# Kernel optimization log

Measured on AMD Instinct MI355X. Metric: run time of the kernel, lower is better.

## Reference

```python
import jax, jax.numpy as jnp
import numpy as np

B, S, D, H = 2, 2048, 1024, 16
DK = D // H
LARGE = 1e9
LN_EPS = 1e-5


def sinusoidal_embeddings(seq_len, d):
    pos = jnp.arange(seq_len, dtype=jnp.float32)[:, None]          # [S,1]
    i = jnp.arange(d // 2, dtype=jnp.float32)[None, :]             # [1,d/2]
    freq = jnp.exp(-(2.0 * i / d) * jnp.log(10000.0))
    ang = pos * freq                                               # [S,d/2]
    pe = jnp.zeros((seq_len, d), dtype=jnp.float32)
    pe = pe.at[:, 0::2].set(jnp.sin(ang))
    pe = pe.at[:, 1::2].set(jnp.cos(ang))
    return pe


def setup_inputs() -> dict:
    key = jax.random.key(0)
    ks = jax.random.split(key, 6)
    sc = 1.0 / np.sqrt(D)
    return {
        "X": jax.random.normal(ks[0], (B, S, D), jnp.float32),
        "W_q": jax.random.normal(ks[1], (D, D), jnp.float32) * sc,
        "W_k": jax.random.normal(ks[2], (D, D), jnp.float32) * sc,
        "W_v": jax.random.normal(ks[3], (D, D), jnp.float32) * sc,
        "W_o": jax.random.normal(ks[4], (D, D), jnp.float32) * sc,
        "alpha": jnp.ones((1, H, S - 1, 1), jnp.float32),
        "ln_scale": jnp.ones((D,), jnp.float32),
        "ln_bias": jnp.zeros((D,), jnp.float32),
    }


def reference(X, W_q, W_k, W_v, W_o, alpha, ln_scale, ln_bias):
    # projections (torch Linear: x @ W.T), split heads -> [B,H,S,dk]
    def proj(W):
        return jnp.einsum('bsd,ed->bse', X, W).reshape(B, S, H, DK).transpose(0, 2, 1, 3)
    Q, K, V = proj(W_q), proj(W_k), proj(W_v)

    # EMA smear on K along sequence
    a = jax.nn.sigmoid(alpha)                                      # [1,H,S-1,1]
    smeared = K[:, :, 1:, :] * a + K[:, :, :-1, :] * (1.0 - a)
    K = jnp.concatenate([K[:, :, 0:1, :], smeared], axis=2)

    # inline sinusoidal positional embeddings added to K and Q
    pe = sinusoidal_embeddings(S, DK)                              # [S,dk]
    K = K + pe
    Q = Q + pe

    mask = jnp.triu(jnp.ones((S, S), jnp.float32), k=1) * (-LARGE)
    scores = jnp.einsum('bhqd,bhkd->bhqk', Q, K) / jnp.sqrt(jnp.float32(DK)) + mask
    weights = jax.nn.softmax(scores, axis=-1)
    attn = jnp.einsum('bhqk,bhkd->bhqd', weights, V)               # [B,H,S,dk]
    attn = attn.transpose(0, 2, 1, 3).reshape(B, S, D)

    Y = jnp.einsum('bsd,ed->bse', attn, W_o) + X

    # LayerNorm
    mu = jnp.mean(Y, axis=-1, keepdims=True)
    var = jnp.mean(jnp.square(Y - mu), axis=-1, keepdims=True)
    Y = (Y - mu) / jnp.sqrt(var + LN_EPS) * ln_scale + ln_bias
    return Y
```

## Files before the change

### kernel.cpp

```cpp
#include <hip/hip_runtime.h>


#define LB __launch_bounds__(256)

typedef unsigned short u16;
typedef __attribute__((ext_vector_type(4))) unsigned short us4;
typedef __attribute__((ext_vector_type(8))) unsigned short us8;
typedef __attribute__((ext_vector_type(8))) __bf16 bf8;
typedef __attribute__((ext_vector_type(4))) float f4;
typedef __attribute__((ext_vector_type(4))) short s4;

static __device__ __forceinline__ float bf2f(u16 h) {
  union { unsigned int u; float f; } c; c.u = ((unsigned int)h) << 16; return c.f;
}
static __device__ __forceinline__ u16 f2bf(float f) {
  union { float f; unsigned int u; } c; c.f = f;
  unsigned int u = c.u + 0x7FFFu + ((c.u >> 16) & 1u);
  return (u16)(u >> 16);
}
static __device__ __forceinline__ float pe_val(int s, int dk) {
  float fr = __expf((float)(dk & ~1) * (-9.210340371976184f / 64.0f));
  float ang = (float)s * fr;
  return (dk & 1) ? __cosf(ang) : __sinf(ang);
}

#if __has_builtin(__builtin_amdgcn_mfma_f32_16x16x16bf16_1k)
static __device__ __forceinline__ f4 mfma16(us4 a, us4 b, f4 c) {
  return __builtin_amdgcn_mfma_f32_16x16x16bf16_1k(
      __builtin_bit_cast(s4, a), __builtin_bit_cast(s4, b), c, 0, 0, 0);
}
#elif __has_builtin(__builtin_amdgcn_mfma_f32_16x16x16_bf16)
typedef __attribute__((ext_vector_type(4))) __bf16 bf4;
static __device__ __forceinline__ f4 mfma16(us4 a, us4 b, f4 c) {
  return __builtin_amdgcn_mfma_f32_16x16x16_bf16(
      __builtin_bit_cast(bf4, a), __builtin_bit_cast(bf4, b), c, 0, 0, 0);
}
#else
static __device__ __forceinline__ f4 mfma16(us4 a, us4 b, f4 c) {
  asm volatile("v_mfma_f32_16x16x16_bf16 %0, %1, %2, %0" : "+v"(c) : "v"(a), "v"(b));
  return c;
}
#endif

#define GLDS(gp, lp) __builtin_amdgcn_global_load_lds( \
    (const __attribute__((address_space(1))) void*)(gp), \
    (__attribute__((address_space(3))) void*)(lp), 16, 0, 0)

__global__ LB void cvt_kernel(const float* __restrict__ X, const float* __restrict__ Wq,
                              const float* __restrict__ Wk, const float* __restrict__ Wv,
                              const float* __restrict__ Wo, u16* __restrict__ Xb,
                              u16* __restrict__ Wcat, u16* __restrict__ Wob) {
  const unsigned t = blockIdx.x * 256 + threadIdx.x;
  const float* src; u16* dst; size_t off;
  if (t < (512u << 10))      { src = X;  dst = Xb;                off = t; }
  else if (t < (640u << 10)) { src = Wq; dst = Wcat;              off = t - (512u << 10); }
  else if (t < (768u << 10)) { src = Wk; dst = Wcat + (1u << 20); off = t - (640u << 10); }
  else if (t < (896u << 10)) { src = Wv; dst = Wcat + (2u << 20); off = t - (768u << 10); }
  else                       { src = Wo; dst = Wob;               off = t - (896u << 10); }
  off *= 8;
  f4 a = *(const f4*)(src + off);
  f4 b = *(const f4*)(src + off + 4);
  us8 o = {f2bf(a[0]), f2bf(a[1]), f2bf(a[2]), f2bf(a[3]),
           f2bf(b[0]), f2bf(b[1]), f2bf(b[2]), f2bf(b[3])};
  *(us8*)(dst + off) = o;
}

static __device__ __forceinline__ void gemm_core(
    const u16* __restrict__ Abase, const u16* __restrict__ Bbase,
    u16* Als, u16* Bls, int m0, int n0, int tid, f4 acc[4][4]) {
  const int w = tid >> 6, lane = tid & 63;
  const int l16 = lane & 15, quad = lane >> 4;
  const int wm = w & 1, wn = w >> 1;
  for (int kk = 0; kk < 1024; kk += 32) {
    __syncthreads();
#pragma unroll
    for (int it = 0; it < 2; it++) {
      int cb = (w * 2 + it) * 64;
      int c = cb + lane;
      int row = c >> 2, kc = c & 3;
      GLDS(Abase + (size_t)(m0 + row) * 1024 + kk + kc * 8, &Als[cb * 8]);
      GLDS(Bbase + (size_t)(n0 + row) * 1024 + kk + kc * 8, &Bls[cb * 8]);
    }
    __syncthreads();
    bf8 af[4], bfr[4];
#pragma unroll
    for (int mt = 0; mt < 4; mt++)
      af[mt] = __builtin_bit_cast(bf8, *(const us8*)(&Als[(wm * 64 + mt * 16 + l16) * 32 + quad * 8]));
#pragma unroll
    for (int nt = 0; nt < 4; nt++)
      bfr[nt] = __builtin_bit_cast(bf8, *(const us8*)(&Bls[(wn * 64 + nt * 16 + l16) * 32 + quad * 8]));
#pragma unroll
    for (int mt = 0; mt < 4; mt++)
#pragma unroll
      for (int nt = 0; nt < 4; nt++)
        acc[mt][nt] = __builtin_amdgcn_mfma_f32_16x16x32_bf16(af[mt], bfr[nt], acc[mt][nt], 0, 0, 0);
  }
}

__global__ LB void gemm_qkv(const u16* __restrict__ Xb, const u16* __restrict__ Wcat,
                            u16* __restrict__ Qb, u16* __restrict__ Kraw,
                            u16* __restrict__ Vp) {
  __shared__ u16 Als[128 * 32];
  __shared__ u16 Bls[128 * 32];
  const int tid = threadIdx.x;
  const int m0 = blockIdx.y * 128, n0 = blockIdx.x * 128;
  f4 acc[4][4];
#pragma unroll
  for (int a = 0; a < 4; a++)
#pragma unroll
    for (int b = 0; b < 4; b++) acc[a][b] = f4{0.f, 0.f, 0.f, 0.f};
  gemm_core(Xb, Wcat, Als, Bls, m0, n0, tid, acc);

  const int w = tid >> 6, lane = tid & 63;
  const int l16 = lane & 15, quad = lane >> 4;
  const int wm = w & 1, wn = w >> 1;
  const int z = blockIdx.x >> 3;
#pragma unroll
  for (int mt = 0; mt < 4; mt++)
#pragma unroll
    for (int nt = 0; nt < 4; nt++)
#pragma unroll
      for (int r = 0; r < 4; r++) {
        int m = m0 + wm * 64 + mt * 16 + quad * 4 + r;
        int nn = (n0 + wn * 64 + nt * 16 + l16) & 1023;
        float v = acc[mt][nt][r];
        int b = m >> 11, s = m & 2047, h = nn >> 6, dk = nn & 63;
        size_t bhoff = (size_t)(b * 16 + h) * (2048 * 64);
        if (z == 0) {
          Qb[bhoff + (size_t)s * 64 + dk] = f2bf(v + pe_val(s, dk));
        } else if (z == 1) {
          Kraw[bhoff + (size_t)s * 64 + dk] = f2bf(v);
        } else {
          int kb = s >> 6, sl = s & 63;
          int t = sl >> 4, Qq = (sl >> 2) & 3, jj = sl & 3;
          int dn = dk >> 4, lv = dk & 15;
          Vp[bhoff + (size_t)kb * 4096 + ((t * 4 + dn) * 64 + Qq * 16 + lv) * 4 + jj] = f2bf(v);
        }
      }
}

__global__ LB void ema_pe(const u16* __restrict__ Kraw, const float* __restrict__ alpha,
                          u16* __restrict__ Kp) {
  int idx = blockIdx.x * 256 + threadIdx.x;
  int b8  = idx & 7;
  int s   = (idx >> 3) & 2047;
  int bh  = idx >> 14;
  int dk8 = b8 * 8;
  size_t base = ((size_t)bh * 2048 + s) * 64 + dk8;
  us8 kc = *(const us8*)(Kraw + base);
  float kv[8];
#pragma unroll
  for (int j = 0; j < 8; j++) kv[j] = bf2f(kc[j]);
  if (s > 0) {
    us8 kp = *(const us8*)(Kraw + base - 64);
    float aa = alpha[(bh & 15) * 2047 + s - 1];
    float a = 1.0f / (1.0f + __expf(-aa));
#pragma unroll
    for (int j = 0; j < 8; j++) kv[j] = kv[j] * a + bf2f(kp[j]) * (1.0f - a);
  }
  us8 o;
#pragma unroll
  for (int j = 0; j < 8; j++) o[j] = f2bf(kv[j] + pe_val(s, dk8 + j));
  int kt16 = s >> 4, c = b8 >> 2, quad = b8 & 3, l16s = s & 15;
  size_t off = (size_t)bh * (2048 * 64) + (size_t)kt16 * 1024 + (c * 64 + quad * 16 + l16s) * 8;
  *(us8*)(Kp + off) = o;
}

template<bool MASK>
static __device__ __forceinline__ void attn_step(
    int kb, const u16* __restrict__ Kt, const u16* __restrict__ Vt,
    const bf8* qf, f4* acc, float& lsum, int lane, int quad, int qrel0) {
  const u16* kbase = Kt + (size_t)kb * 4096;
  const u16* vbase = Vt + (size_t)kb * 4096;
  f4 sc[4];
#pragma unroll
  for (int t = 0; t < 4; t++) sc[t] = f4{0.f, 0.f, 0.f, 0.f};
#pragma unroll
  for (int t = 0; t < 4; t++)
#pragma unroll
    for (int c = 0; c < 2; c++) {
      bf8 kf = __builtin_bit_cast(bf8, *(const us8*)(kbase + (t * 2 + c) * 512 + lane * 8));
      sc[t] = __builtin_amdgcn_mfma_f32_16x16x32_bf16(kf, qf[c], sc[t], 0, 0, 0);
    }
  us4 pf[4];
#pragma unroll
  for (int t = 0; t < 4; t++) {
#pragma unroll
    for (int r = 0; r < 4; r++) {
      float s = sc[t][r];
      if (MASK && (t * 16 + quad * 4 + r > qrel0)) s = -1e30f;
      float p = __expf(__builtin_fmaf(s, 0.125f, -22.18070977791825f));
      lsum += p;
      pf[t][r] = f2bf(p);
    }
#pragma unroll
    for (int dn = 0; dn < 4; dn++) {
      us4 vf = *(const us4*)(vbase + ((t * 4 + dn) * 64 + lane) * 4);
      acc[dn] = mfma16(vf, pf[t], acc[dn]);
    }
  }
}

__global__ LB void attn_kernel(const u16* __restrict__ Qb, const u16* __restrict__ Kp,
                               const u16* __restrict__ Vp, u16* __restrict__ Ab) {
  const int tid = threadIdx.x, w = tid >> 6, lane = tid & 63;
  const int l16 = lane & 15, quad = lane >> 4;
  const int idx = blockIdx.x;
  const int bh = idx & 31;
  const int q0 = (31 - (idx >> 5)) * 64;
  const int qw = q0 + w * 16;
  const size_t bhoff = (size_t)bh * (2048 * 64);
  const u16* Kt = Kp + bhoff;
  const u16* Vt = Vp + bhoff;

  bf8 qf[2];
#pragma unroll
  for (int c = 0; c < 2; c++)
    qf[c] = __builtin_bit_cast(bf8, *(const us8*)(Qb + bhoff + (size_t)(qw + l16) * 64 + c * 32 + quad * 8));

  f4 acc[4];
#pragma unroll
  for (int dn = 0; dn < 4; dn++) acc[dn] = f4{0.f, 0.f, 0.f, 0.f};
  float lsum = 0.f;

  const int nfull = (qw + 1) >> 6;
  for (int kb = 0; kb < nfull; kb++)
    attn_step<false>(kb, Kt, Vt, qf, acc, lsum, lane, quad, 0);
  attn_step<true>(nfull, Kt, Vt, qf, acc, lsum, lane, quad, qw + l16 - nfull * 64);

  lsum += __shfl_xor(lsum, 16, 64);
  lsum += __shfl_xor(lsum, 32, 64);
  float rinv = 1.0f / lsum;

  const int b = bh >> 4, h = bh & 15;
  const int q = qw + l16;
  u16* orow = Ab + ((size_t)(b * 2048 + q)) * 1024 + h * 64;
#pragma unroll
  for (int dn = 0; dn < 4; dn++) {
    us4 o = {f2bf(acc[dn][0] * rinv), f2bf(acc[dn][1] * rinv),
             f2bf(acc[dn][2] * rinv), f2bf(acc[dn][3] * rinv)};
    *(us4*)(orow + dn * 16 + quad * 4) = o;
  }
}

__global__ LB void gemm_out(const u16* __restrict__ Ab, const u16* __restrict__ Wob,
                            const float* __restrict__ X, float* __restrict__ Yp) {
  __shared__ u16 Als[128 * 32];
  __shared__ u16 Bls[128 * 32];
  const int tid = threadIdx.x;
  const int m0 = blockIdx.y * 128, n0 = blockIdx.x * 128;
  f4 acc[4][4];
#pragma unroll
  for (int a = 0; a < 4; a++)
#pragma unroll
    for (int b = 0; b < 4; b++) acc[a][b] = f4{0.f, 0.f, 0.f, 0.f};
  gemm_core(Ab, Wob, Als, Bls, m0, n0, tid, acc);

  const int w = tid >> 6, lane = tid & 63;
  const int l16 = lane & 15, quad = lane >> 4;
  const int wm = w & 1, wn = w >> 1;
#pragma unroll
  for (int mt = 0; mt < 4; mt++)
#pragma unroll
    for (int nt = 0; nt < 4; nt++)
#pragma unroll
      for (int r = 0; r < 4; r++) {
        int m = m0 + wm * 64 + mt * 16 + quad * 4 + r;
        int n = n0 + wn * 64 + nt * 16 + l16;
        size_t o = (size_t)m * 1024 + n;
        Yp[o] = acc[mt][nt][r] + X[o];
      }
}

__global__ LB void ln_kernel(const float* __restrict__ Y, const float* __restrict__ g,
                             const float* __restrict__ bta, float* __restrict__ out) {
  __shared__ float ls[4], lsq[4];
  const int row = blockIdx.x, tid = threadIdx.x;
  const int w = tid >> 6, lane = tid & 63;
  f4 v = *(const f4*)(Y + (size_t)row * 1024 + tid * 4);
  float s  = v[0] + v[1] + v[2] + v[3];
  float sq = v[0] * v[0] + v[1] * v[1] + v[2] * v[2] + v[3] * v[3];
#pragma unroll
  for (int d = 1; d < 64; d <<= 1) { s += __shfl_xor(s, d, 64); sq += __shfl_xor(sq, d, 64); }
  if (lane == 0) { ls[w] = s; lsq[w] = sq; }
  __syncthreads();
  s  = ls[0] + ls[1] + ls[2] + ls[3];
  sq = lsq[0] + lsq[1] + lsq[2] + lsq[3];
  float mu  = s * (1.0f / 1024.0f);
  float var = sq * (1.0f / 1024.0f) - mu * mu;
  float rs  = rsqrtf(var + 1e-5f);
  f4 o;
#pragma unroll
  for (int j = 0; j < 4; j++) {
    int col = tid * 4 + j;
    o[j] = (v[j] - mu) * rs * g[col] + bta[col];
  }
  *(f4*)(out + (size_t)row * 1024 + tid * 4) = o;
}

extern "C" void kernel_launch(void* const* d_in, const int* in_sizes, int n_in,
                              void* d_out, int out_size, void* d_ws, size_t ws_size,
                              hipStream_t stream) {
  (void)in_sizes; (void)n_in; (void)out_size; (void)ws_size;
  const float* X  = (const float*)d_in[0];
  const float* Wq = (const float*)d_in[1];
  const float* Wk = (const float*)d_in[2];
  const float* Wv = (const float*)d_in[3];
  const float* Wo = (const float*)d_in[4];
  const float* al = (const float*)d_in[5];
  const float* g  = (const float*)d_in[6];
  const float* bt = (const float*)d_in[7];

  char* ws = (char*)d_ws;
  float* Yp   = (float*)(ws);
  u16*   Xb   = (u16*)(ws + ((size_t)16 << 20));
  u16*   Wcat = (u16*)(ws + ((size_t)24 << 20));
  u16*   Wob  = (u16*)(ws + ((size_t)30 << 20));
  u16*   Qb   = (u16*)(ws + ((size_t)32 << 20));
  u16*   Kraw = (u16*)(ws + ((size_t)40 << 20));
  u16*   Ab   = (u16*)(ws + ((size_t)40 << 20));
  u16*   Kp   = (u16*)(ws + ((size_t)48 << 20));
  u16*   Vp   = (u16*)(ws + ((size_t)56 << 20));

  cvt_kernel<<<dim3(4096), 256, 0, stream>>>(X, Wq, Wk, Wv, Wo, Xb, Wcat, Wob);
  gemm_qkv<<<dim3(24, 32), 256, 0, stream>>>(Xb, Wcat, Qb, Kraw, Vp);
  ema_pe<<<dim3(2048), 256, 0, stream>>>(Kraw, al, Kp);
  attn_kernel<<<dim3(1024), 256, 0, stream>>>(Qb, Kp, Vp, Ab);
  gemm_out<<<dim3(8, 32), 256, 0, stream>>>(Ab, Wob, X, Yp);
  ln_kernel<<<dim3(4096), 256, 0, stream>>>(Yp, g, bt, (float*)d_out);
}
```

Measured before the change: 219.8 us.

## Process two 16-row query tiles per wave in attention to reuse K/V loads

```diff
diff --git a/kernel.cpp b/kernel.cpp
--- a/kernel.cpp
+++ b/kernel.cpp
@@ -169,36 +169,43 @@
 template<bool MASK>
 static __device__ __forceinline__ void attn_step(
     int kb, const u16* __restrict__ Kt, const u16* __restrict__ Vt,
-    const bf8* qf, f4* acc, float& lsum, int lane, int quad, int qrel0) {
+    const bf8 qf[2][2], f4 acc[2][4], float* lsum, int lane, int quad, int qrel) {
   const u16* kbase = Kt + (size_t)kb * 4096;
   const u16* vbase = Vt + (size_t)kb * 4096;
-  f4 sc[4];
-#pragma unroll
-  for (int t = 0; t < 4; t++) sc[t] = f4{0.f, 0.f, 0.f, 0.f};
+  f4 sc[2][4];
+#pragma unroll
+  for (int h = 0; h < 2; h++)
+#pragma unroll
+    for (int t = 0; t < 4; t++) sc[h][t] = f4{0.f, 0.f, 0.f, 0.f};
 #pragma unroll
   for (int t = 0; t < 4; t++)
 #pragma unroll
     for (int c = 0; c < 2; c++) {
       bf8 kf = __builtin_bit_cast(bf8, *(const us8*)(kbase + (t * 2 + c) * 512 + lane * 8));
-      sc[t] = __builtin_amdgcn_mfma_f32_16x16x32_bf16(kf, qf[c], sc[t], 0, 0, 0);
+      sc[0][t] = __builtin_amdgcn_mfma_f32_16x16x32_bf16(kf, qf[0][c], sc[0][t], 0, 0, 0);
+      sc[1][t] = __builtin_amdgcn_mfma_f32_16x16x32_bf16(kf, qf[1][c], sc[1][t], 0, 0, 0);
     }
-  us4 pf[4];
-#pragma unroll
-  for (int t = 0; t < 4; t++) {
-#pragma unroll
-    for (int r = 0; r < 4; r++) {
-      float s = sc[t][r];
-      if (MASK && (t * 16 + quad * 4 + r > qrel0)) s = -1e30f;
-      float p = __expf(__builtin_fmaf(s, 0.125f, -22.18070977791825f));
-      lsum += p;
-      pf[t][r] = f2bf(p);
-    }
+  us4 pf[2][4];
+#pragma unroll
+  for (int h = 0; h < 2; h++)
+#pragma unroll
+    for (int t = 0; t < 4; t++)
+#pragma unroll
+      for (int r = 0; r < 4; r++) {
+        float s = sc[h][t][r];
+        if (MASK && (t * 16 + quad * 4 + r > qrel + h * 16)) s = -1e30f;
+        float p = exp2f(__builtin_fmaf(s, 0.18033688011112042f, -32.0f));
+        lsum[h] += p;
+        pf[h][t][r] = f2bf(p);
+      }
+#pragma unroll
+  for (int t = 0; t < 4; t++)
 #pragma unroll
     for (int dn = 0; dn < 4; dn++) {
       us4 vf = *(const us4*)(vbase + ((t * 4 + dn) * 64 + lane) * 4);
-      acc[dn] = mfma16(vf, pf[t], acc[dn]);
+      acc[0][dn] = mfma16(vf, pf[0][t], acc[0][dn]);
+      acc[1][dn] = mfma16(vf, pf[1][t], acc[1][dn]);
     }
-  }
 }
 
 __global__ LB void attn_kernel(const u16* __restrict__ Qb, const u16* __restrict__ Kp,
@@ -207,39 +214,52 @@
   const int l16 = lane & 15, quad = lane >> 4;
   const int idx = blockIdx.x;
   const int bh = idx & 31;
-  const int q0 = (31 - (idx >> 5)) * 64;
-  const int qw = q0 + w * 16;
+  const int q0 = (15 - (idx >> 5)) * 128;
+  const int qw = q0 + w * 32;
   const size_t bhoff = (size_t)bh * (2048 * 64);
   const u16* Kt = Kp + bhoff;
   const u16* Vt = Vp + bhoff;
 
-  bf8 qf[2];
-#pragma unroll
-  for (int c = 0; c < 2; c++)
-    qf[c] = __builtin_bit_cast(bf8, *(const us8*)(Qb + bhoff + (size_t)(qw + l16) * 64 + c * 32 + quad * 8));
-
-  f4 acc[4];
-#pragma unroll
-  for (int dn = 0; dn < 4; dn++) acc[dn] = f4{0.f, 0.f, 0.f, 0.f};
-  float lsum = 0.f;
+  bf8 qf[2][2];
+#pragma unroll
+  for (int h = 0; h < 2; h++)
+#pragma unroll
+    for (int c = 0; c < 2; c++)
+      qf[h][c] = __builtin_bit_cast(bf8,
+          *(const us8*)(Qb + bhoff + (size_t)(qw + h * 16 + l16) * 64 + c * 32 + quad * 8));
+
+  f4 acc[2][4];
+#pragma unroll
+  for (int h = 0; h < 2; h++)
+#pragma unroll
+    for (int dn = 0; dn < 4; dn++) acc[h][dn] = f4{0.f, 0.f, 0.f, 0.f};
+  float lsum[2] = {0.f, 0.f};
 
   const int nfull = (qw + 1) >> 6;
+  const int kbmax = (qw + 31) >> 6;
   for (int kb = 0; kb < nfull; kb++)
     attn_step<false>(kb, Kt, Vt, qf, acc, lsum, lane, quad, 0);
-  attn_step<true>(nfull, Kt, Vt, qf, acc, lsum, lane, quad, qw + l16 - nfull * 64);
-
-  lsum += __shfl_xor(lsum, 16, 64);
-  lsum += __shfl_xor(lsum, 32, 64);
-  float rinv = 1.0f / lsum;
-
-  const int b = bh >> 4, h = bh & 15;
-  const int q = qw + l16;
-  u16* orow = Ab + ((size_t)(b * 2048 + q)) * 1024 + h * 64;
-#pragma unroll
-  for (int dn = 0; dn < 4; dn++) {
-    us4 o = {f2bf(acc[dn][0] * rinv), f2bf(acc[dn][1] * rinv),
-             f2bf(acc[dn][2] * rinv), f2bf(acc[dn][3] * rinv)};
-    *(us4*)(orow + dn * 16 + quad * 4) = o;
+  for (int kb = nfull; kb <= kbmax; kb++)
+    attn_step<true>(kb, Kt, Vt, qf, acc, lsum, lane, quad, qw + l16 - kb * 64);
+
+#pragma unroll
+  for (int h = 0; h < 2; h++) {
+    lsum[h] += __shfl_xor(lsum[h], 16, 64);
+    lsum[h] += __shfl_xor(lsum[h], 32, 64);
+  }
+
+  const int b = bh >> 4, hd = bh & 15;
+#pragma unroll
+  for (int h = 0; h < 2; h++) {
+    float rinv = 1.0f / lsum[h];
+    const int q = qw + h * 16 + l16;
+    u16* orow = Ab + ((size_t)(b * 2048 + q)) * 1024 + hd * 64;
+#pragma unroll
+    for (int dn = 0; dn < 4; dn++) {
+      us4 o = {f2bf(acc[h][dn][0] * rinv), f2bf(acc[h][dn][1] * rinv),
+               f2bf(acc[h][dn][2] * rinv), f2bf(acc[h][dn][3] * rinv)};
+      *(us4*)(orow + dn * 16 + quad * 4) = o;
+    }
   }
 }
 
@@ -325,7 +345,7 @@
   cvt_kernel<<<dim3(4096), 256, 0, stream>>>(X, Wq, Wk, Wv, Wo, Xb, Wcat, Wob);
   gemm_qkv<<<dim3(24, 32), 256, 0, stream>>>(Xb, Wcat, Qb, Kraw, Vp);
   ema_pe<<<dim3(2048), 256, 0, stream>>>(Kraw, al, Kp);
-  attn_kernel<<<dim3(1024), 256, 0, stream>>>(Qb, Kp, Vp, Ab);
+  attn_kernel<<<dim3(512), 256, 0, stream>>>(Qb, Kp, Vp, Ab);
   gemm_out<<<dim3(8, 32), 256, 0, stream>>>(Ab, Wob, X, Yp);
   ln_kernel<<<dim3(4096), 256, 0, stream>>>(Yp, g, bt, (float*)d_out);
 }
```

After: 365.3 us. 1.66x slower.

## Split attention key range across wave pairs and combine partials in LDS

Applied to the files above, without the earlier changes.

```diff
diff --git a/kernel.cpp b/kernel.cpp
--- a/kernel.cpp
+++ b/kernel.cpp
@@ -2,8 +2,11 @@
 
 
 #define LB __launch_bounds__(256)
+#define LB8 __launch_bounds__(256, 8)
 
 typedef unsigned short u16;
+typedef unsigned int u32;
+typedef __attribute__((ext_vector_type(2))) unsigned int u32x2;
 typedef __attribute__((ext_vector_type(4))) unsigned short us4;
 typedef __attribute__((ext_vector_type(8))) unsigned short us8;
 typedef __attribute__((ext_vector_type(8))) __bf16 bf8;
@@ -18,6 +21,19 @@
   unsigned int u = c.u + 0x7FFFu + ((c.u >> 16) & 1u);
   return (u16)(u >> 16);
 }
+#if __has_builtin(__builtin_amdgcn_cvt_pk_bf16_f32)
+typedef __attribute__((ext_vector_type(2))) __bf16 bf2v;
+static __device__ __forceinline__ us4 pk_bf16x4(f4 v) {
+  bf2v lo = __builtin_amdgcn_cvt_pk_bf16_f32(v[0], v[1]);
+  bf2v hi = __builtin_amdgcn_cvt_pk_bf16_f32(v[2], v[3]);
+  u32x2 r = {__builtin_bit_cast(u32, lo), __builtin_bit_cast(u32, hi)};
+  return __builtin_bit_cast(us4, r);
+}
+#else
+static __device__ __forceinline__ us4 pk_bf16x4(f4 v) {
+  return us4{f2bf(v[0]), f2bf(v[1]), f2bf(v[2]), f2bf(v[3])};
+}
+#endif
 static __device__ __forceinline__ float pe_val(int s, int dk) {
   float fr = __expf((float)(dk & ~1) * (-9.210340371976184f / 64.0f));
   float ang = (float)s * fr;
@@ -185,30 +201,37 @@
   us4 pf[4];
 #pragma unroll
   for (int t = 0; t < 4; t++) {
+    f4 pv;
 #pragma unroll
     for (int r = 0; r < 4; r++) {
       float s = sc[t][r];
       if (MASK && (t * 16 + quad * 4 + r > qrel0)) s = -1e30f;
-      float p = __expf(__builtin_fmaf(s, 0.125f, -22.18070977791825f));
+      float p = exp2f(__builtin_fmaf(s, 0.18033688011112042f, -32.0f));
       lsum += p;
-      pf[t][r] = f2bf(p);
-    }
+      pv[r] = p;
+    }
+    pf[t] = pk_bf16x4(pv);
+  }
+#pragma unroll
+  for (int t = 0; t < 4; t++)
 #pragma unroll
     for (int dn = 0; dn < 4; dn++) {
       us4 vf = *(const us4*)(vbase + ((t * 4 + dn) * 64 + lane) * 4);
       acc[dn] = mfma16(vf, pf[t], acc[dn]);
     }
-  }
-}
-
-__global__ LB void attn_kernel(const u16* __restrict__ Qb, const u16* __restrict__ Kp,
-                               const u16* __restrict__ Vp, u16* __restrict__ Ab) {
+}
+
+__global__ LB8 void attn_kernel(const u16* __restrict__ Qb, const u16* __restrict__ Kp,
+                                const u16* __restrict__ Vp, u16* __restrict__ Ab) {
+  __shared__ float comb[2][64][20];
   const int tid = threadIdx.x, w = tid >> 6, lane = tid & 63;
   const int l16 = lane & 15, quad = lane >> 4;
   const int idx = blockIdx.x;
   const int bh = idx & 31;
-  const int q0 = (31 - (idx >> 5)) * 64;
-  const int qw = q0 + w * 16;
+  const int qg = 63 - (idx >> 5);
+  const int qt = w & 1;
+  const int h2 = w >> 1;
+  const int qw = qg * 32 + qt * 16;
   const size_t bhoff = (size_t)bh * (2048 * 64);
   const u16* Kt = Kp + bhoff;
   const u16* Vt = Vp + bhoff;
@@ -223,23 +246,44 @@
   for (int dn = 0; dn < 4; dn++) acc[dn] = f4{0.f, 0.f, 0.f, 0.f};
   float lsum = 0.f;
 
-  const int nfull = (qw + 1) >> 6;
-  for (int kb = 0; kb < nfull; kb++)
+  const int T  = (qw >> 6) + 1;
+  const int Th = (T + 1) >> 1;
+  const int kbs = h2 ? Th : 0;
+  const int kbe = h2 ? T : Th;
+  const int e_un = (kbe < T - 1) ? kbe : (T - 1);
+  for (int kb = kbs; kb < e_un; kb++)
     attn_step<false>(kb, Kt, Vt, qf, acc, lsum, lane, quad, 0);
-  attn_step<true>(nfull, Kt, Vt, qf, acc, lsum, lane, quad, qw + l16 - nfull * 64);
-
-  lsum += __shfl_xor(lsum, 16, 64);
-  lsum += __shfl_xor(lsum, 32, 64);
-  float rinv = 1.0f / lsum;
-
-  const int b = bh >> 4, h = bh & 15;
-  const int q = qw + l16;
-  u16* orow = Ab + ((size_t)(b * 2048 + q)) * 1024 + h * 64;
-#pragma unroll
-  for (int dn = 0; dn < 4; dn++) {
-    us4 o = {f2bf(acc[dn][0] * rinv), f2bf(acc[dn][1] * rinv),
-             f2bf(acc[dn][2] * rinv), f2bf(acc[dn][3] * rinv)};
-    *(us4*)(orow + dn * 16 + quad * 4) = o;
+  if (kbe == T && kbe > kbs)
+    attn_step<true>(T - 1, Kt, Vt, qf, acc, lsum, lane, quad, qw + l16 - (T - 1) * 64);
+
+  if (h2) {
+    float* d = &comb[qt][lane][0];
+    *(f4*)(d)      = acc[0];
+    *(f4*)(d + 4)  = acc[1];
+    *(f4*)(d + 8)  = acc[2];
+    *(f4*)(d + 12) = acc[3];
+    d[16] = lsum;
+  }
+  __syncthreads();
+  if (!h2) {
+    const float* s = &comb[qt][lane][0];
+    acc[0] += *(const f4*)(s);
+    acc[1] += *(const f4*)(s + 4);
+    acc[2] += *(const f4*)(s + 8);
+    acc[3] += *(const f4*)(s + 12);
+    lsum += s[16];
+    lsum += __shfl_xor(lsum, 16, 64);
+    lsum += __shfl_xor(lsum, 32, 64);
+    float rinv = 1.0f / lsum;
+    const int b = bh >> 4, h = bh & 15;
+    const int q = qw + l16;
+    u16* orow = Ab + ((size_t)(b * 2048 + q)) * 1024 + h * 64;
+#pragma unroll
+    for (int dn = 0; dn < 4; dn++) {
+      us4 o = pk_bf16x4(f4{acc[dn][0] * rinv, acc[dn][1] * rinv,
+                           acc[dn][2] * rinv, acc[dn][3] * rinv});
+      *(us4*)(orow + dn * 16 + quad * 4) = o;
+    }
   }
 }
 
@@ -325,7 +369,7 @@
   cvt_kernel<<<dim3(4096), 256, 0, stream>>>(X, Wq, Wk, Wv, Wo, Xb, Wcat, Wob);
   gemm_qkv<<<dim3(24, 32), 256, 0, stream>>>(Xb, Wcat, Qb, Kraw, Vp);
   ema_pe<<<dim3(2048), 256, 0, stream>>>(Kraw, al, Kp);
-  attn_kernel<<<dim3(1024), 256, 0, stream>>>(Qb, Kp, Vp, Ab);
+  attn_kernel<<<dim3(2048), 256, 0, stream>>>(Qb, Kp, Vp, Ab);
   gemm_out<<<dim3(8, 32), 256, 0, stream>>>(Ab, Wob, X, Yp);
   ln_kernel<<<dim3(4096), 256, 0, stream>>>(Yp, g, bt, (float*)d_out);
 }
```

Result: slower. 250.2 us (+13.8%).
